# Performance work log

Hardware: AMD Instinct MI355X
Metric: run time of the kernel (lower is better)

Reference implementation:

```python
import jax, jax.numpy as jnp
import numpy as np
import math

D_MODEL = 1024
EXPAND = 2
D_INNER = EXPAND * D_MODEL        # 2048
HEADDIM = 64
NHEADS = D_INNER // HEADDIM       # 32
D_STATE = 128
D_CONV = 4
CHUNK = 128
SEQLEN = 4096
BATCH = 1                         # bidirectional merge in forward hard-codes batch=1
CONV_DIM = D_INNER + 2 * (2 * D_STATE)            # 2560
D_IN_PROJ = 2 * D_INNER + 2 * (2 * D_STATE) + 2 * NHEADS  # 4672
EPS = 1e-5


def silu(x):
    return x * jax.nn.sigmoid(x)


def segsum_exp(a):
    """exp(segsum(a)): out[..., i, j] = exp(sum_{k=j+1..i} a[..., k]) for i>=j else 0."""
    T = a.shape[-1]
    m1 = jnp.tril(jnp.ones((T, T), bool), -1)
    s = jnp.cumsum(jnp.where(m1, a[..., :, None], 0.0), axis=-2)
    m0 = jnp.tril(jnp.ones((T, T), bool))
    return jnp.where(m0, jnp.exp(jnp.where(m0, s, 0.0)), 0.0)


def ssd(x, A, B, C, chunk):
    """x:(b,L,h,p) A:(b,L,h) B,C:(b,L,n) (head dim of size 1 squeezed). L % chunk == 0."""
    b, L, h, p = x.shape
    c = L // chunk
    x = x.reshape(b, c, chunk, h, p)
    A = A.reshape(b, c, chunk, h).transpose(0, 3, 1, 2)   # (b,h,c,l)
    B = B.reshape(b, c, chunk, -1)
    C = C.reshape(b, c, chunk, -1)
    A_cs = jnp.cumsum(A, axis=-1)                          # (b,h,c,l)
    Lmat = segsum_exp(A)                                   # (b,h,c,l,l)
    # intra-chunk (diagonal block) outputs
    Y_diag = jnp.einsum('bcln,bcsn,bhcls,bcshp->bclhp', C, B, Lmat, x)
    # per-chunk states
    decay_states = jnp.exp(A_cs[..., -1:] - A_cs)          # (b,h,c,l)
    states = jnp.einsum('bcln,bhcl,bclhp->bchpn', B, decay_states, x)
    states = jnp.concatenate([jnp.zeros_like(states[:, :1]), states], axis=1)
    # inter-chunk recurrence via segsum over chunk boundaries
    decay_chunk = segsum_exp(jnp.pad(A_cs[..., -1], ((0, 0), (0, 0), (1, 0))))  # (b,h,c+1,c+1)
    new_states = jnp.einsum('bhzc,bchpn->bzhpn', decay_chunk, states)
    states, final_state = new_states[:, :-1], new_states[:, -1]
    Y_off = jnp.einsum('bcln,bchpn,bhcl->bclhp', C, states, jnp.exp(A_cs))
    Y = (Y_diag + Y_off).reshape(b, L, h, p)
    return Y, final_state


def setup_inputs() -> dict:
    key = jax.random.key(0)
    ks = jax.random.split(key, 8)
    s = 0.02
    u = jax.random.normal(ks[0], (BATCH, SEQLEN, D_MODEL), jnp.float32)
    in_proj_w = jax.random.normal(ks[1], (D_IN_PROJ, D_MODEL), jnp.float32) * s
    conv_w = jax.random.normal(ks[2], (CONV_DIM, 1, D_CONV), jnp.float32) * (1.0 / math.sqrt(D_CONV))
    conv_b = jnp.zeros((CONV_DIM,), jnp.float32)
    dt = jnp.exp(jax.random.uniform(ks[3], (NHEADS,)) * (math.log(0.1) - math.log(0.001)) + math.log(0.001))
    dt = jnp.clip(dt, 1e-4)
    dt_bias = dt + jnp.log(-jnp.expm1(-dt))
    A_log = jnp.log(jax.random.uniform(ks[4], (NHEADS,), minval=1.0, maxval=16.0))
    D = jnp.ones((NHEADS,), jnp.float32)
    fc_D_w = jax.random.normal(ks[5], (NHEADS, D_INNER), jnp.float32) * s
    norm_w = jnp.ones((D_INNER,), jnp.float32)
    out_proj_w = jax.random.normal(ks[6], (D_MODEL, D_INNER), jnp.float32) * s
    return dict(u=u, in_proj_w=in_proj_w, conv_w=conv_w, conv_b=conv_b, dt_bias=dt_bias,
                A_log=A_log, D=D, fc_D_w=fc_D_w, norm_w=norm_w, out_proj_w=out_proj_w)


def reference(u, in_proj_w, conv_w, conv_b, dt_bias, A_log, D, fc_D_w, norm_w, out_proj_w):
    b, l, _ = u.shape
    zxbcdt = u @ in_proj_w.T                               # (b,l,D_IN_PROJ)
    z = zxbcdt[..., :D_INNER]
    xBC = zxbcdt[..., D_INNER:D_INNER + CONV_DIM]
    dt = zxbcdt[..., D_INNER + CONV_DIM:]                  # (b,l,2*nheads)
    # fwd heads + time-reversed bwd heads stacked on batch dim
    dt = jnp.concatenate([dt[..., :NHEADS], jnp.flip(dt[..., NHEADS:], axis=1)], axis=0)
    dt = jax.nn.softplus(dt + dt_bias)                     # (2b,l,nheads)
    # depthwise causal conv1d + silu
    xc = jnp.transpose(xBC, (0, 2, 1))                     # (b,CONV_DIM,l)
    xc = jax.lax.conv_general_dilated(xc, conv_w, (1,), [(D_CONV - 1, 0)],
                                      feature_group_count=CONV_DIM,
                                      dimension_numbers=('NCH', 'OIH', 'NCH'))
    xc = xc + conv_b[None, :, None]
    xBC = silu(jnp.transpose(xc, (0, 2, 1)))               # (b,l,CONV_DIM)
    x = xBC[..., :D_INNER]
    BC = xBC[..., D_INNER:]
    x_og = x
    x2 = jnp.concatenate([x, jnp.flip(x, 1)], axis=0)      # (2b,l,d_inner)
    BC = jnp.concatenate([BC[..., :2 * D_STATE], jnp.flip(BC[..., 2 * D_STATE:], 1)], axis=0)
    B = BC[..., :D_STATE]
    C = BC[..., D_STATE:]
    xh = x2.reshape(2 * b, l, NHEADS, HEADDIM)
    A = -jnp.exp(A_log)
    Y, final_state = ssd(xh * dt[..., None], A * dt, B, C, CHUNK)
    y = Y + xh * D[:, None]
    y = y.reshape(2 * b, l, D_INNER)
    # torch.roll(shift=1, dim=1) then zero first step == shift right with zero pad
    y = jnp.concatenate([jnp.zeros_like(y[:, :1]), y[:, :-1]], axis=1)
    y_fw, y_bw = y[:b], jnp.flip(y[b:], 1)
    fd = x_og @ fc_D_w.T + D                               # F.linear(x_og, fc_D.weight, bias=D)
    y = y_fw + y_bw + x_og * jnp.repeat(fd, HEADDIM, axis=-1)
    # gated RMSNorm
    yg = y * silu(z)
    yn = yg * jax.lax.rsqrt(jnp.mean(yg * yg, axis=-1, keepdims=True) + EPS) * norm_w
    return yn @ out_proj_w.T
```

## Files before the change

kernel.cpp:

```cpp
#include <hip/hip_runtime.h>
#include <hip/hip_bf16.h>
#include <math.h>

#define L_SEQ   4096
#define DMODEL  1024
#define DINNER  2048
#define NHEADS  32
#define HEADDIM 64
#define DSTATE  128
#define NCHUNK  32
#define CHUNKL  128
#define CONVDIM 2560
#define DPROJ   4672
#define NPAD1   4736
#define NSPLIT  4096

typedef __hip_bfloat16 bf16;
__device__ __forceinline__ float b2f(bf16 x) { return __bfloat162float(x); }
__device__ __forceinline__ bf16 f2b(float x) { return __float2bfloat16(x); }
__device__ __forceinline__ float sh2f(short s) {
  return __uint_as_float(((unsigned int)(unsigned short)s) << 16);
}
__device__ __forceinline__ short f2bs(float x) {
  bf16 t = __float2bfloat16(x);
  return *reinterpret_cast<short*>(&t);
}

typedef __attribute__((ext_vector_type(8))) short bf16x8v;
typedef __attribute__((ext_vector_type(4))) float f32x4v;

__device__ __forceinline__ float dot8(bf16x8v x, float4 w0, float4 w1) {
  return sh2f(x[0]) * w0.x + sh2f(x[1]) * w0.y + sh2f(x[2]) * w0.z + sh2f(x[3]) * w0.w +
         sh2f(x[4]) * w1.x + sh2f(x[5]) * w1.y + sh2f(x[6]) * w1.z + sh2f(x[7]) * w1.w;
}


__global__ __launch_bounds__(256) void cast2_kernel(
    const float* __restrict__ u, const float* __restrict__ w1,
    bf16* __restrict__ u_bf, bf16* __restrict__ w1_bf) {
  const int NU = (L_SEQ * DMODEL) / 256;
  int bid = blockIdx.x;
  if (bid < NU) {
    int i = bid * 256 + threadIdx.x;
    u_bf[i] = f2b(u[i]);
  } else {
    int i = (bid - NU) * 256 + threadIdx.x;
    w1_bf[i] = (i < DPROJ * DMODEL) ? f2b(w1[i]) : f2b(0.f);
  }
}

__global__ __launch_bounds__(256) void cast_kernel(
    const float* __restrict__ src, bf16* __restrict__ dst, int n_src, int n_tot) {
  int i = blockIdx.x * 256 + threadIdx.x;
  if (i < n_tot) dst[i] = (i < n_src) ? f2b(src[i]) : f2b(0.f);
}

#define G1_K  1024
#define G1_GN 16
#define G1_NT (G1_K / 64)

__global__ __launch_bounds__(512, 2) void gemm1_8ph(
    const bf16* __restrict__ A, const bf16* __restrict__ B, bf16* __restrict__ C) {
  __shared__ bf16 Al[2][2][8192];
  __shared__ bf16 Bl[2][2][8192];
  const int tid = threadIdx.x;
  const int lane = tid & 63;
  const int w = tid >> 6;
  const int wm = w >> 2;
  const int wn = w & 3;
  const int bm = (blockIdx.x / G1_GN) * 256;
  const int bn = (blockIdx.x % G1_GN) * 256;
  const int scol = ((lane & 3) ^ (((lane >> 5) & 1) << 1)) * 8;
  const int cin = ((lane >> 4) * 8) ^ (((lane >> 3) & 1) << 4);
  const int r16 = lane & 15;
  const bf16* Ag = A + (size_t)bm * G1_K;
  const bf16* Bg = B + (size_t)bn * G1_K;

  auto stage = [&](int mat, int tt, int hf) {
    const bf16* g = (mat ? Bg : Ag)
        + (size_t)(hf * 128 + (w >> 1) * 16 + (lane >> 2)) * G1_K
        + tt * 64 + (w & 1) * 32 + scol;
    bf16* d0 = mat ? &Bl[tt & 1][hf][0] : &Al[tt & 1][hf][0];
    __builtin_amdgcn_global_load_lds(
        (const __attribute__((address_space(1))) void*)g,
        (__attribute__((address_space(3))) void*)(d0 + w * 512), 16, 0, 0);
    __builtin_amdgcn_global_load_lds(
        (const __attribute__((address_space(1))) void*)(g + (size_t)64 * G1_K),
        (__attribute__((address_space(3))) void*)(d0 + (8 + w) * 512), 16, 0, 0);
  };

  f32x4v acc[8][4];
#pragma unroll
  for (int i = 0; i < 8; i++)
#pragma unroll
    for (int j = 0; j < 4; j++) acc[i][j] = (f32x4v){0.f, 0.f, 0.f, 0.f};

  stage(0, 0, 0); stage(0, 0, 1); stage(1, 0, 0); stage(1, 0, 1);
  stage(0, 1, 0); stage(0, 1, 1); stage(1, 1, 0);
  asm volatile("s_waitcnt vmcnt(6)" ::: "memory");
  __builtin_amdgcn_s_barrier();
  __builtin_amdgcn_sched_barrier(0);

#pragma unroll 2
  for (int t = 0; t < G1_NT; ++t) {
    const int slot = t & 1;
    const bf16* Ah = &Al[slot][wm][0];
    const bf16* Bh = &Bl[slot][wn >> 1][0];
    const int brb = (wn & 1) * 4;
    bf16x8v a[4][2], b[4][2];
#pragma unroll
    for (int i = 0; i < 4; i++) {
      a[i][0] = *(const bf16x8v*)&Ah[(i * 2 + 0) * 512 + r16 * 32 + cin];
      a[i][1] = *(const bf16x8v*)&Ah[(i * 2 + 1) * 512 + r16 * 32 + cin];
    }
#pragma unroll
    for (int j = 0; j < 2; j++) {
      b[j][0] = *(const bf16x8v*)&Bh[((brb + j) * 2 + 0) * 512 + r16 * 32 + cin];
      b[j][1] = *(const bf16x8v*)&Bh[((brb + j) * 2 + 1) * 512 + r16 * 32 + cin];
    }
    if (t + 1 < G1_NT) stage(1, t + 1, 1);
    __builtin_amdgcn_s_barrier();
    asm volatile("s_waitcnt lgkmcnt(0)" ::: "memory");
    __builtin_amdgcn_s_setprio(1);
#pragma unroll
    for (int i = 0; i < 4; i++)
#pragma unroll
      for (int j = 0; j < 2; j++) {
        acc[i][j] = __builtin_amdgcn_mfma_f32_16x16x32_bf16(a[i][0], b[j][0], acc[i][j], 0, 0, 0);
        acc[i][j] = __builtin_amdgcn_mfma_f32_16x16x32_bf16(a[i][1], b[j][1], acc[i][j], 0, 0, 0);
      }
    __builtin_amdgcn_s_setprio(0);
    __builtin_amdgcn_s_barrier();
#pragma unroll
    for (int j = 2; j < 4; j++) {
      b[j][0] = *(const bf16x8v*)&Bh[((brb + j) * 2 + 0) * 512 + r16 * 32 + cin];
      b[j][1] = *(const bf16x8v*)&Bh[((brb + j) * 2 + 1) * 512 + r16 * 32 + cin];
    }
    __builtin_amdgcn_s_barrier();
    asm volatile("s_waitcnt lgkmcnt(0)" ::: "memory");
    __builtin_amdgcn_s_setprio(1);
#pragma unroll
    for (int i = 0; i < 4; i++)
#pragma unroll
      for (int j = 2; j < 4; j++) {
        acc[i][j] = __builtin_amdgcn_mfma_f32_16x16x32_bf16(a[i][0], b[j][0], acc[i][j], 0, 0, 0);
        acc[i][j] = __builtin_amdgcn_mfma_f32_16x16x32_bf16(a[i][1], b[j][1], acc[i][j], 0, 0, 0);
      }
    __builtin_amdgcn_s_setprio(0);
    __builtin_amdgcn_s_barrier();
#pragma unroll
    for (int i = 0; i < 4; i++) {
      a[i][0] = *(const bf16x8v*)&Ah[((4 + i) * 2 + 0) * 512 + r16 * 32 + cin];
      a[i][1] = *(const bf16x8v*)&Ah[((4 + i) * 2 + 1) * 512 + r16 * 32 + cin];
    }
    if (t + 2 < G1_NT) stage(1, t + 2, 0);
    __builtin_amdgcn_s_barrier();
    asm volatile("s_waitcnt lgkmcnt(0)" ::: "memory");
    __builtin_amdgcn_s_setprio(1);
#pragma unroll
    for (int i = 0; i < 4; i++)
#pragma unroll
      for (int j = 2; j < 4; j++) {
        acc[4 + i][j] = __builtin_amdgcn_mfma_f32_16x16x32_bf16(a[i][0], b[j][0], acc[4 + i][j], 0, 0, 0);
        acc[4 + i][j] = __builtin_amdgcn_mfma_f32_16x16x32_bf16(a[i][1], b[j][1], acc[4 + i][j], 0, 0, 0);
      }
    __builtin_amdgcn_s_setprio(0);
    __builtin_amdgcn_s_barrier();
    if (t + 2 < G1_NT) { stage(0, t + 2, 0); stage(0, t + 2, 1); }
    __builtin_amdgcn_s_barrier();
    __builtin_amdgcn_s_setprio(1);
#pragma unroll
    for (int i = 0; i < 4; i++)
#pragma unroll
      for (int j = 0; j < 2; j++) {
        acc[4 + i][j] = __builtin_amdgcn_mfma_f32_16x16x32_bf16(a[i][0], b[j][0], acc[4 + i][j], 0, 0, 0);
        acc[4 + i][j] = __builtin_amdgcn_mfma_f32_16x16x32_bf16(a[i][1], b[j][1], acc[4 + i][j], 0, 0, 0);
      }
    __builtin_amdgcn_s_setprio(0);
    if (t < G1_NT - 2)       asm volatile("s_waitcnt vmcnt(6)" ::: "memory");
    else if (t == G1_NT - 2) asm volatile("s_waitcnt vmcnt(0)" ::: "memory");
    __builtin_amdgcn_s_barrier();
    __builtin_amdgcn_sched_barrier(0);
  }

  const int quad = lane >> 4;
  const int cn = lane & 15;
#pragma unroll
  for (int i = 0; i < 8; i++)
#pragma unroll
    for (int j = 0; j < 4; j++) {
      int col = bn + wn * 64 + j * 16 + cn;
      if (col < DPROJ) {
#pragma unroll
        for (int r = 0; r < 4; r++) {
          int row = bm + wm * 128 + i * 16 + quad * 4 + r;
          C[(size_t)row * DPROJ + col] = f2b(acc[i][j][r]);
        }
      }
    }
}

template <typename TC>
__global__ __launch_bounds__(256) void gemm_mfma(
    const bf16* __restrict__ A, int lda,
    const bf16* __restrict__ B, int ldb,
    TC* __restrict__ C, int ldc,
    int N, int K, int gridM, int gridN, int swz) {
  __shared__ short As[128][32];
  __shared__ short Bs[128][32];
  int tid = threadIdx.x;
  int lane = tid & 63;
  int w = tid >> 6;
  int wr = w >> 1, wc = w & 1;
  int bid = blockIdx.x;
  int bm, bn;
  if (swz) {
    int mst = gridM >> 3;
    int xk = bid & 7, q = bid >> 3;
    bm = (xk + 8 * (q % mst)) * 128;
    bn = (q / mst) * 128;
  } else {
    bm = (bid / gridN) * 128;
    bn = (bid % gridN) * 128;
  }
  f32x4v acc[4][4];
#pragma unroll
  for (int i = 0; i < 4; i++)
#pragma unroll
    for (int j = 0; j < 4; j++) acc[i][j] = (f32x4v){0.f, 0.f, 0.f, 0.f};

  const bf16* Ab = A + (size_t)(bm + w * 32 + (lane >> 2)) * lda + (lane & 3) * 8;
  const bf16* Bb = B + (size_t)(bn + w * 32 + (lane >> 2)) * ldb + (lane & 3) * 8;

  for (int k0 = 0; k0 < K; k0 += 32) {
    __builtin_amdgcn_global_load_lds(
        (const __attribute__((address_space(1))) void*)(Ab + k0),
        (__attribute__((address_space(3))) void*)&As[w * 32][0], 16, 0, 0);
    __builtin_amdgcn_global_load_lds(
        (const __attribute__((address_space(1))) void*)(Ab + (size_t)16 * lda + k0),
        (__attribute__((address_space(3))) void*)&As[w * 32 + 16][0], 16, 0, 0);
    __builtin_amdgcn_global_load_lds(
        (const __attribute__((address_space(1))) void*)(Bb + k0),
        (__attribute__((address_space(3))) void*)&Bs[w * 32][0], 16, 0, 0);
    __builtin_amdgcn_global_load_lds(
        (const __attribute__((address_space(1))) void*)(Bb + (size_t)16 * ldb + k0),
        (__attribute__((address_space(3))) void*)&Bs[w * 32 + 16][0], 16, 0, 0);
    __syncthreads();
    bf16x8v af[4], bv[4];
#pragma unroll
    for (int i = 0; i < 4; i++)
      af[i] = *(const bf16x8v*)&As[wr * 64 + i * 16 + (lane & 15)][(lane >> 4) * 8];
#pragma unroll
    for (int j = 0; j < 4; j++)
      bv[j] = *(const bf16x8v*)&Bs[wc * 64 + j * 16 + (lane & 15)][(lane >> 4) * 8];
#pragma unroll
    for (int i = 0; i < 4; i++)
#pragma unroll
      for (int j = 0; j < 4; j++)
        acc[i][j] = __builtin_amdgcn_mfma_f32_16x16x32_bf16(af[i], bv[j], acc[i][j], 0, 0, 0);
    __syncthreads();
  }
  int quad = lane >> 4;
  int cn = lane & 15;
#pragma unroll
  for (int i = 0; i < 4; i++) {
#pragma unroll
    for (int j = 0; j < 4; j++) {
      int col = bn + wc * 64 + j * 16 + cn;
      if (col < N) {
#pragma unroll
        for (int r = 0; r < 4; r++) {
          int row = bm + wr * 64 + i * 16 + quad * 4 + r;
          float v = acc[i][j][r];
          if constexpr (sizeof(TC) == 2) C[(size_t)row * ldc + col] = f2b(v);
          else                           C[(size_t)row * ldc + col] = v;
        }
      }
    }
  }
}

__global__ __launch_bounds__(256) void fc_kernel(
    const bf16* __restrict__ xbc, const float* __restrict__ Wf,
    const float* __restrict__ Dp, float* __restrict__ fd) {
  int lane = threadIdx.x & 63;
  int w = threadIdx.x >> 6;
  int t0 = blockIdx.x * 4;
  int h = lane & 31;
  int g = lane >> 5;
  int k0 = w * 512 + g * 256;
  const float* wr = Wf + (size_t)h * DINNER + k0;
  const bf16* xr = xbc + (size_t)t0 * CONVDIM + k0;
  float a0 = 0.f, a1 = 0.f, a2 = 0.f, a3 = 0.f;
#pragma unroll 4
  for (int k = 0; k < 256; k += 8) {
    float4 w0 = *(const float4*)(wr + k);
    float4 w1 = *(const float4*)(wr + k + 4);
    bf16x8v x0 = *(const bf16x8v*)(xr + k);
    bf16x8v x1 = *(const bf16x8v*)(xr + CONVDIM + k);
    bf16x8v x2 = *(const bf16x8v*)(xr + 2 * CONVDIM + k);
    bf16x8v x3 = *(const bf16x8v*)(xr + 3 * CONVDIM + k);
    a0 += dot8(x0, w0, w1);
    a1 += dot8(x1, w0, w1);
    a2 += dot8(x2, w0, w1);
    a3 += dot8(x3, w0, w1);
  }
  a0 += __shfl_down(a0, 32);
  a1 += __shfl_down(a1, 32);
  a2 += __shfl_down(a2, 32);
  a3 += __shfl_down(a3, 32);
  __shared__ float red[4][4][32];
  if (lane < 32) {
    red[w][0][h] = a0; red[w][1][h] = a1; red[w][2][h] = a2; red[w][3][h] = a3;
  }
  __syncthreads();
  int tid = threadIdx.x;
  if (tid < 128) {
    int tt = tid >> 5;
    int hh = tid & 31;
    float s = red[0][tt][hh] + red[1][tt][hh] + red[2][tt][hh] + red[3][tt][hh];
    fd[(t0 + tt) * NHEADS + hh] = s + Dp[hh];
  }
}

#define CONV_BLOCKS ((L_SEQ / 4) * CONVDIM / 256)
__global__ __launch_bounds__(256) void conv_dt_kernel(
    const bf16* __restrict__ zx, const float* __restrict__ conv_w,
    const float* __restrict__ conv_b, bf16* __restrict__ xbc,
    const float* __restrict__ dt_bias, float* __restrict__ dt2) {
  int bid = blockIdx.x;
  if (bid < CONV_BLOCKS) {
    int idx = bid * 256 + threadIdx.x;
    int ch = idx % CONVDIM;
    int t0 = (idx / CONVDIM) * 4;
    const bf16* col = zx + DINNER + ch;
    float w0 = conv_w[ch * 4 + 0], w1 = conv_w[ch * 4 + 1];
    float w2 = conv_w[ch * 4 + 2], w3 = conv_w[ch * 4 + 3];
    float bsv = conv_b[ch];
    float x[7];
#pragma unroll
    for (int i = 0; i < 7; i++) {
      int t = t0 - 3 + i;
      x[i] = (t >= 0) ? b2f(col[(size_t)t * DPROJ]) : 0.f;
    }
#pragma unroll
    for (int j = 0; j < 4; j++) {
      float acc = bsv + w0 * x[j] + w1 * x[j + 1] + w2 * x[j + 2] + w3 * x[j + 3];
      xbc[(size_t)(t0 + j) * CONVDIM + ch] = f2b(acc / (1.f + __expf(-acc)));
    }
  } else {
    int idx = (bid - CONV_BLOCKS) * 256 + threadIdx.x;
    int h = idx % NHEADS;
    int t = (idx / NHEADS) % L_SEQ;
    int b = idx / (NHEADS * L_SEQ);
    float v;
    if (b == 0) v = b2f(zx[(size_t)t * DPROJ + 4608 + h]);
    else        v = b2f(zx[(size_t)(L_SEQ - 1 - t) * DPROJ + 4608 + NHEADS + h]);
    v += dt_bias[h];
    dt2[idx] = (v > 20.f) ? v : log1pf(expf(v));
  }
}

__global__ __launch_bounds__(256) void gmat_kernel(
    const bf16* __restrict__ xbc, bf16* __restrict__ G) {
  __shared__ bf16 Cs[32][136];
  __shared__ bf16 Bs[128][136];
  int blk = blockIdx.x;
  int quarter = blk & 3;
  int bc = blk >> 2;
  int b = bc / NCHUNK, c = bc % NCHUNK;
  int l0 = quarter * 32;
  int tid = threadIdx.x;
  int lane = tid & 63;
  int w = tid >> 6;
  int bofs = b ? 2304 : 2048;
  int cofs = b ? 2432 : 2176;
  for (int o = tid; o < CHUNKL * DSTATE / 8; o += 256) {
    int s = o >> 4;
    int n8 = (o & 15) * 8;
    int t = b ? (L_SEQ - 1 - (c * CHUNKL + s)) : (c * CHUNKL + s);
    *(bf16x8v*)&Bs[s][n8] = *(const bf16x8v*)&xbc[(size_t)t * CONVDIM + bofs + n8];
  }
  for (int o = tid; o < 32 * DSTATE / 8; o += 256) {
    int l = o >> 4;
    int n8 = (o & 15) * 8;
    int t = b ? (L_SEQ - 1 - (c * CHUNKL + l0 + l)) : (c * CHUNKL + l0 + l);
    *(bf16x8v*)&Cs[l][n8] = *(const bf16x8v*)&xbc[(size_t)t * CONVDIM + cofs + n8];
  }
  __syncthreads();
  if (w > quarter) return;
  f32x4v acc[2][2];
#pragma unroll
  for (int i = 0; i < 2; i++)
#pragma unroll
    for (int j = 0; j < 2; j++) acc[i][j] = (f32x4v){0.f, 0.f, 0.f, 0.f};
#pragma unroll
  for (int k0 = 0; k0 < 128; k0 += 32) {
    bf16x8v a0 = *(const bf16x8v*)&Cs[(lane & 15)][(lane >> 4) * 8 + k0];
    bf16x8v a1 = *(const bf16x8v*)&Cs[16 + (lane & 15)][(lane >> 4) * 8 + k0];
#pragma unroll
    for (int j = 0; j < 2; j++) {
      bf16x8v bv = *(const bf16x8v*)&Bs[(2 * w + j) * 16 + (lane & 15)][(lane >> 4) * 8 + k0];
      acc[0][j] = __builtin_amdgcn_mfma_f32_16x16x32_bf16(a0, bv, acc[0][j], 0, 0, 0);
      acc[1][j] = __builtin_amdgcn_mfma_f32_16x16x32_bf16(a1, bv, acc[1][j], 0, 0, 0);
    }
  }
  int quad = lane >> 4, cn = lane & 15;
  bf16* Gb = G + (size_t)bc * CHUNKL * CHUNKL;
#pragma unroll
  for (int i = 0; i < 2; i++)
#pragma unroll
    for (int j = 0; j < 2; j++)
#pragma unroll
      for (int r = 0; r < 4; r++) {
        int l = l0 + i * 16 + quad * 4 + r;
        int s = (2 * w + j) * 16 + cn;
        Gb[l * CHUNKL + s] = f2b(acc[i][j][r]);
      }
}

__global__ __launch_bounds__(256) void chunk_kernel(
    const bf16* __restrict__ xbc, const float* __restrict__ dt2,
    const float* __restrict__ A_log,
    bf16* __restrict__ states, float* __restrict__ csum) {
  int gid = blockIdx.x;
  int h = gid % NHEADS;
  int bc = gid / NHEADS;
  int c = bc % NCHUNK, b = bc / NCHUNK;
  int tid = threadIdx.x;
  int lane = tid & 63;
  int w = tid >> 6;
  __shared__ bf16 BdT[128][136];
  __shared__ bf16 xdtT[64][136];
  __shared__ float acs[CHUNKL];
  __shared__ float dtl[CHUNKL];
  __shared__ float decays[CHUNKL];
  if (tid < CHUNKL)
    dtl[tid] = dt2[((size_t)b * L_SEQ + c * CHUNKL + tid) * NHEADS + h];
  __syncthreads();
  if (tid == 0) {
    float Ah = -__expf(A_log[h]);
    float s = 0.f;
    for (int l = 0; l < CHUNKL; l++) { s += Ah * dtl[l]; acs[l] = s; }
    csum[gid] = __expf(s);
  }
  __syncthreads();
  if (tid < CHUNKL) decays[tid] = __expf(acs[CHUNKL - 1] - acs[tid]);
  for (int o = tid; o < CHUNKL * HEADDIM / 8; o += 256) {
    int s = o & 127;
    int p8 = (o >> 7) * 8;
    int t = b ? (L_SEQ - 1 - (c * CHUNKL + s)) : (c * CHUNKL + s);
    bf16x8v xv = *(const bf16x8v*)&xbc[(size_t)t * CONVDIM + h * HEADDIM + p8];
    float d = dtl[s];
#pragma unroll
    for (int j = 0; j < 8; j++) xdtT[p8 + j][s] = f2b(sh2f(xv[j]) * d);
  }
  __syncthreads();
  for (int o = tid; o < CHUNKL * CHUNKL / 8; o += 256) {
    int l = o & 127;
    int n8 = (o >> 7) * 8;
    int t = b ? (L_SEQ - 1 - (c * CHUNKL + l)) : (c * CHUNKL + l);
    bf16x8v bv = *(const bf16x8v*)&xbc[(size_t)t * CONVDIM + (b ? 2304 : 2048) + n8];
    float d = decays[l];
#pragma unroll
    for (int j = 0; j < 8; j++) BdT[n8 + j][l] = f2b(sh2f(bv[j]) * d);
  }
  __syncthreads();
  f32x4v accS[8];
#pragma unroll
  for (int j = 0; j < 8; j++) accS[j] = (f32x4v){0.f, 0.f, 0.f, 0.f};
#pragma unroll
  for (int k0 = 0; k0 < 128; k0 += 32) {
    bf16x8v av = *(const bf16x8v*)&xdtT[w * 16 + (lane & 15)][(lane >> 4) * 8 + k0];
#pragma unroll
    for (int j = 0; j < 8; j++) {
      bf16x8v bv = *(const bf16x8v*)&BdT[j * 16 + (lane & 15)][(lane >> 4) * 8 + k0];
      accS[j] = __builtin_amdgcn_mfma_f32_16x16x32_bf16(av, bv, accS[j], 0, 0, 0);
    }
  }
  int quad = lane >> 4, cn = lane & 15;
  bf16* st = states + (size_t)gid * (HEADDIM * DSTATE);
#pragma unroll
  for (int j = 0; j < 8; j++)
#pragma unroll
    for (int r = 0; r < 4; r++) {
      int p = w * 16 + quad * 4 + r;
      int n = j * 16 + cn;
      st[p * DSTATE + n] = f2b(accS[j][r]);
    }
}

__global__ __launch_bounds__(256) void scan_kernel(
    bf16* __restrict__ states, const float* __restrict__ csum) {
  int idx = blockIdx.x * 256 + threadIdx.x;
  int n = idx % DSTATE;
  int p = (idx / DSTATE) % HEADDIM;
  int h = (idx / (DSTATE * HEADDIM)) % NHEADS;
  int b = idx / (DSTATE * HEADDIM * NHEADS);
  size_t base = ((size_t)(b * NCHUNK) * NHEADS + h) * (HEADDIM * DSTATE) + p * DSTATE + n;
  const size_t cstride = (size_t)NHEADS * HEADDIM * DSTATE;
  float tmp[NCHUNK], cv[NCHUNK];
#pragma unroll
  for (int c = 0; c < NCHUNK; c++) tmp[c] = b2f(states[base + c * cstride]);
#pragma unroll
  for (int c = 0; c < NCHUNK; c++) cv[c] = csum[(b * NCHUNK + c) * NHEADS + h];
  float S = 0.f;
#pragma unroll
  for (int c = 0; c < NCHUNK; c++) {
    states[base + c * cstride] = f2b(S);
    S = cv[c] * S + tmp[c];
  }
}

__global__ __launch_bounds__(256) void yoff_kernel(
    const bf16* __restrict__ xbc, const float* __restrict__ dt2,
    const float* __restrict__ A_log, const bf16* __restrict__ G,
    const bf16* __restrict__ states, const float* __restrict__ Dp,
    bf16* __restrict__ Y) {
  int gid = blockIdx.x;
  int h = gid % NHEADS;
  int bc = gid / NHEADS;
  int c = bc % NCHUNK, b = bc / NCHUNK;
  int tid = threadIdx.x;
  int lane = tid & 63;
  int w = tid >> 6;
  __shared__ bf16 WB[128][136];
  __shared__ bf16 SX[64][136];
  __shared__ float acs[CHUNKL];
  __shared__ float dtl[CHUNKL];
  __shared__ float eAl[CHUNKL];
  if (tid < CHUNKL)
    dtl[tid] = dt2[((size_t)b * L_SEQ + c * CHUNKL + tid) * NHEADS + h];
  __syncthreads();
  if (tid == 0) {
    float Ah = -__expf(A_log[h]);
    float s = 0.f;
    for (int l = 0; l < CHUNKL; l++) { s += Ah * dtl[l]; acs[l] = s; }
  }
  __syncthreads();
  if (tid < CHUNKL) eAl[tid] = __expf(acs[tid]);
  for (int o = tid; o < CHUNKL * HEADDIM / 8; o += 256) {
    int s = o & 127;
    int p8 = (o >> 7) * 8;
    int t = b ? (L_SEQ - 1 - (c * CHUNKL + s)) : (c * CHUNKL + s);
    bf16x8v xv = *(const bf16x8v*)&xbc[(size_t)t * CONVDIM + h * HEADDIM + p8];
    float d = dtl[s];
#pragma unroll
    for (int j = 0; j < 8; j++) SX[p8 + j][s] = f2b(sh2f(xv[j]) * d);
  }
  {
    const bf16* Gb = G + (size_t)bc * CHUNKL * CHUNKL;
    for (int o = tid; o < CHUNKL * CHUNKL / 8; o += 256) {
      int l = o >> 4;
      int s8 = (o & 15) * 8;
      bf16x8v g = *(const bf16x8v*)&Gb[l * CHUNKL + s8];
      float al = acs[l];
      bf16x8v wv;
#pragma unroll
      for (int j = 0; j < 8; j++) {
        int s = s8 + j;
        float e = (s <= l) ? sh2f(g[j]) * __expf(al - acs[s]) : 0.f;
        wv[j] = f2bs(e);
      }
      *(bf16x8v*)&WB[l][s8] = wv;
    }
  }
  __syncthreads();
  f32x4v accY[2][4];
#pragma unroll
  for (int i = 0; i < 2; i++)
#pragma unroll
    for (int j = 0; j < 4; j++) accY[i][j] = (f32x4v){0.f, 0.f, 0.f, 0.f};
#pragma unroll
  for (int k0 = 0; k0 < 128; k0 += 32) {
    bf16x8v a0 = *(const bf16x8v*)&WB[w * 32 + (lane & 15)][(lane >> 4) * 8 + k0];
    bf16x8v a1 = *(const bf16x8v*)&WB[w * 32 + 16 + (lane & 15)][(lane >> 4) * 8 + k0];
#pragma unroll
    for (int j = 0; j < 4; j++) {
      bf16x8v bv = *(const bf16x8v*)&SX[j * 16 + (lane & 15)][(lane >> 4) * 8 + k0];
      accY[0][j] = __builtin_amdgcn_mfma_f32_16x16x32_bf16(a0, bv, accY[0][j], 0, 0, 0);
      accY[1][j] = __builtin_amdgcn_mfma_f32_16x16x32_bf16(a1, bv, accY[1][j], 0, 0, 0);
    }
  }
  __syncthreads();
  {
    int cofs = b ? 2432 : 2176;
    for (int o = tid; o < CHUNKL * DSTATE / 8; o += 256) {
      int l = o >> 4;
      int n8 = (o & 15) * 8;
      int t = b ? (L_SEQ - 1 - (c * CHUNKL + l)) : (c * CHUNKL + l);
      bf16x8v cv = *(const bf16x8v*)&xbc[(size_t)t * CONVDIM + cofs + n8];
      float e = eAl[l];
      bf16x8v ov;
#pragma unroll
      for (int j = 0; j < 8; j++) ov[j] = f2bs(sh2f(cv[j]) * e);
      *(bf16x8v*)&WB[l][n8] = ov;
    }
    const bf16* stp = states + (size_t)gid * (HEADDIM * DSTATE);
    for (int o = tid; o < HEADDIM * DSTATE / 8; o += 256) {
      int p = o >> 4;
      int n8 = (o & 15) * 8;
      *(bf16x8v*)&SX[p][n8] = *(const bf16x8v*)&stp[o * 8];
    }
  }
  __syncthreads();
#pragma unroll
  for (int k0 = 0; k0 < 128; k0 += 32) {
    bf16x8v a0 = *(const bf16x8v*)&WB[w * 32 + (lane & 15)][(lane >> 4) * 8 + k0];
    bf16x8v a1 = *(const bf16x8v*)&WB[w * 32 + 16 + (lane & 15)][(lane >> 4) * 8 + k0];
#pragma unroll
    for (int j = 0; j < 4; j++) {
      bf16x8v bv = *(const bf16x8v*)&SX[j * 16 + (lane & 15)][(lane >> 4) * 8 + k0];
      accY[0][j] = __builtin_amdgcn_mfma_f32_16x16x32_bf16(a0, bv, accY[0][j], 0, 0, 0);
      accY[1][j] = __builtin_amdgcn_mfma_f32_16x16x32_bf16(a1, bv, accY[1][j], 0, 0, 0);
    }
  }
  int quad = lane >> 4, cn = lane & 15;
  float Dh = Dp[h];
#pragma unroll
  for (int i = 0; i < 2; i++)
#pragma unroll
    for (int j = 0; j < 4; j++)
#pragma unroll
      for (int r = 0; r < 4; r++) {
        int l = w * 32 + i * 16 + quad * 4 + r;
        int p = j * 16 + cn;
        int t = b ? (L_SEQ - 1 - (c * CHUNKL + l)) : (c * CHUNKL + l);
        float xv = b2f(xbc[(size_t)t * CONVDIM + h * HEADDIM + p]);
        size_t yi = ((size_t)b * L_SEQ + c * CHUNKL + l) * DINNER + h * HEADDIM + p;
        Y[yi] = f2b(accY[i][j][r] + xv * Dh);
      }
}

__global__ __launch_bounds__(256) void combine_kernel(
    const bf16* __restrict__ Y, const bf16* __restrict__ xbc,
    const bf16* __restrict__ zx, const float* __restrict__ fd,
    const float* __restrict__ norm_w, bf16* __restrict__ yn) {
  int t = blockIdx.x;
  int tid = threadIdx.x;
  int j8 = tid * 8;
  float yf[8], yb[8];
#pragma unroll
  for (int j = 0; j < 8; j++) { yf[j] = 0.f; yb[j] = 0.f; }
  if (t >= 1) {
    bf16x8v v = *(const bf16x8v*)&Y[(size_t)(t - 1) * DINNER + j8];
#pragma unroll
    for (int j = 0; j < 8; j++) yf[j] = sh2f(v[j]);
  }
  if (t <= L_SEQ - 2) {
    bf16x8v v = *(const bf16x8v*)&Y[((size_t)L_SEQ + (L_SEQ - 2 - t)) * DINNER + j8];
#pragma unroll
    for (int j = 0; j < 8; j++) yb[j] = sh2f(v[j]);
  }
  bf16x8v xogv = *(const bf16x8v*)&xbc[(size_t)t * CONVDIM + j8];
  bf16x8v zv = *(const bf16x8v*)&zx[(size_t)t * DPROJ + j8];
  float fdv = fd[t * NHEADS + (j8 >> 6)];
  float yg[8];
  float ss = 0.f;
#pragma unroll
  for (int j = 0; j < 8; j++) {
    float y = yf[j] + yb[j] + sh2f(xogv[j]) * fdv;
    float z = sh2f(zv[j]);
    float g = y * (z / (1.f + __expf(-z)));
    yg[j] = g;
    ss += g * g;
  }
#pragma unroll
  for (int off = 32; off > 0; off >>= 1) ss += __shfl_down(ss, off);
  __shared__ float red[4];
  if ((tid & 63) == 0) red[tid >> 6] = ss;
  __syncthreads();
  float tot = red[0] + red[1] + red[2] + red[3];
  float scale = rsqrtf(tot / (float)DINNER + 1e-5f);
  float4 nw0 = *(const float4*)&norm_w[j8];
  float4 nw1 = *(const float4*)&norm_w[j8 + 4];
  bf16x8v ov;
  ov[0] = f2bs(yg[0] * scale * nw0.x);
  ov[1] = f2bs(yg[1] * scale * nw0.y);
  ov[2] = f2bs(yg[2] * scale * nw0.z);
  ov[3] = f2bs(yg[3] * scale * nw0.w);
  ov[4] = f2bs(yg[4] * scale * nw1.x);
  ov[5] = f2bs(yg[5] * scale * nw1.y);
  ov[6] = f2bs(yg[6] * scale * nw1.z);
  ov[7] = f2bs(yg[7] * scale * nw1.w);
  *(bf16x8v*)&yn[(size_t)t * DINNER + j8] = ov;
}

extern "C" void kernel_launch(void* const* d_in, const int* in_sizes, int n_in,
                              void* d_out, int out_size, void* d_ws, size_t ws_size,
                              hipStream_t stream) {
  const float* u         = (const float*)d_in[0];
  const float* in_proj_w = (const float*)d_in[1];
  const float* conv_w    = (const float*)d_in[2];
  const float* conv_b    = (const float*)d_in[3];
  const float* dt_bias   = (const float*)d_in[4];
  const float* A_log     = (const float*)d_in[5];
  const float* Dp        = (const float*)d_in[6];
  const float* fc_D_w    = (const float*)d_in[7];
  const float* norm_w    = (const float*)d_in[8];
  const float* out_proj_w= (const float*)d_in[9];
  float* out = (float*)d_out;

  char* base = (char*)d_ws;
  bf16*  zx  = (bf16*)base;  base += (size_t)L_SEQ * DPROJ * 2;
  bf16*  xbc = (bf16*)base;  base += (size_t)L_SEQ * CONVDIM * 2;
  float* dt2 = (float*)base; base += (size_t)2 * L_SEQ * NHEADS * 4;
  bf16*  G   = (bf16*)base;  base += (size_t)2 * NCHUNK * CHUNKL * CHUNKL * 4;
  bf16*  Yb  = (bf16*)base;  base += (size_t)2 * L_SEQ * DINNER * 4;
  bf16*  stb = (bf16*)base;  base += (size_t)2 * NCHUNK * NHEADS * HEADDIM * DSTATE * 4;
  float* cs  = (float*)base; base += (size_t)2 * NCHUNK * NHEADS * 4;
  bf16*  u_bf   = (bf16*)Yb;
  bf16*  w1p_bf = (bf16*)((char*)Yb + 9437184);
  bf16*  w2_bf  = (bf16*)G;
  bf16*  yn     = (bf16*)stb;
  float* fd     = (float*)((char*)stb + 33554432);

  cast2_kernel<<<(L_SEQ * DMODEL + NPAD1 * DMODEL) / 256, 256, 0, stream>>>(
      u, in_proj_w, u_bf, w1p_bf);
  gemm1_8ph<<<(L_SEQ / 256) * G1_GN, 512, 0, stream>>>(u_bf, w1p_bf, zx);
  gemm_mfma<bf16><<<(L_SEQ / 128) * ((NPAD1 - NSPLIT) / 128), 256, 0, stream>>>(
      u_bf, DMODEL, w1p_bf + (size_t)NSPLIT * DMODEL, DMODEL,
      zx + NSPLIT, DPROJ, DPROJ - NSPLIT, DMODEL,
      L_SEQ / 128, (NPAD1 - NSPLIT) / 128, 0);
  conv_dt_kernel<<<CONV_BLOCKS + (2 * L_SEQ * NHEADS) / 256, 256, 0, stream>>>(
      zx, conv_w, conv_b, xbc, dt_bias, dt2);
  gmat_kernel<<<2 * NCHUNK * 4, 256, 0, stream>>>(xbc, G);
  chunk_kernel<<<2 * NCHUNK * NHEADS, 256, 0, stream>>>(
      xbc, dt2, A_log, stb, cs);
  scan_kernel<<<(2 * NHEADS * HEADDIM * DSTATE) / 256, 256, 0, stream>>>(stb, cs);
  yoff_kernel<<<2 * NCHUNK * NHEADS, 256, 0, stream>>>(
      xbc, dt2, A_log, G, stb, Dp, Yb);
  cast_kernel<<<(DMODEL * DINNER + 255) / 256, 256, 0, stream>>>(
      out_proj_w, w2_bf, DMODEL * DINNER, DMODEL * DINNER);
  fc_kernel<<<L_SEQ / 4, 256, 0, stream>>>(xbc, fc_D_w, Dp, fd);
  combine_kernel<<<L_SEQ, 256, 0, stream>>>(Yb, xbc, zx, fd, norm_w, yn);
  gemm_mfma<float><<<(L_SEQ / 128) * (DMODEL / 128), 256, 0, stream>>>(
      yn, DINNER, w2_bf, DINNER, out, DMODEL, DMODEL, DINNER,
      L_SEQ / 128, DMODEL / 128, 1);
}
```

Baseline: 403.5 us.

## Split yoff kernel rows across two blocks, skip masked causal tiles, parallel cumsum

The yoff kernel is launched with twice as many blocks, each handling 64 of the 128 chunk rows, which halves the WB shared buffer and the per-wave accumulators. The causal (lower-triangular) structure is used to skip loading G and computing exponentials for fully masked 8-wide segments, and to break out of the intra-chunk MFMA loop once k passes the wave's last row. The serial single-thread cumulative sum over dt is replaced by a wavefront shuffle-based prefix scan. In exchange, each block still reloads the dt vector, the SX tile and the state tile, so that global traffic is duplicated across the two halves.

```diff
diff --git a/kernel.cpp b/kernel.cpp
--- a/kernel.cpp
+++ b/kernel.cpp
@@ -517,14 +517,17 @@
     const float* __restrict__ A_log, const bf16* __restrict__ G,
     const bf16* __restrict__ states, const float* __restrict__ Dp,
     bf16* __restrict__ Y) {
-  int gid = blockIdx.x;
+  int blk = blockIdx.x;
+  int half = blk & 1;
+  int gid = blk >> 1;
   int h = gid % NHEADS;
   int bc = gid / NHEADS;
   int c = bc % NCHUNK, b = bc / NCHUNK;
+  int l0 = half * 64;
   int tid = threadIdx.x;
   int lane = tid & 63;
   int w = tid >> 6;
-  __shared__ bf16 WB[128][136];
+  __shared__ bf16 WB[64][136];
   __shared__ bf16 SX[64][136];
   __shared__ float acs[CHUNKL];
   __shared__ float dtl[CHUNKL];
@@ -532,10 +535,18 @@
   if (tid < CHUNKL)
     dtl[tid] = dt2[((size_t)b * L_SEQ + c * CHUNKL + tid) * NHEADS + h];
   __syncthreads();
-  if (tid == 0) {
+  if (tid < 64) {
     float Ah = -__expf(A_log[h]);
-    float s = 0.f;
-    for (int l = 0; l < CHUNKL; l++) { s += Ah * dtl[l]; acs[l] = s; }
+    float v0 = Ah * dtl[2 * tid];
+    float v1 = Ah * dtl[2 * tid + 1];
+    float s = v0 + v1;
+#pragma unroll
+    for (int off = 1; off < 64; off <<= 1) {
+      float t = __shfl_up(s, off);
+      if (tid >= off) s += t;
+    }
+    acs[2 * tid]     = s - v1;
+    acs[2 * tid + 1] = s;
   }
   __syncthreads();
   if (tid < CHUNKL) eAl[tid] = __expf(acs[tid]);
@@ -550,43 +561,48 @@
   }
   {
     const bf16* Gb = G + (size_t)bc * CHUNKL * CHUNKL;
-    for (int o = tid; o < CHUNKL * CHUNKL / 8; o += 256) {
-      int l = o >> 4;
+    for (int o = tid; o < 64 * CHUNKL / 8; o += 256) {
+      int ll = o >> 4;
+      int l = l0 + ll;
       int s8 = (o & 15) * 8;
-      bf16x8v g = *(const bf16x8v*)&Gb[l * CHUNKL + s8];
-      float al = acs[l];
       bf16x8v wv;
-#pragma unroll
-      for (int j = 0; j < 8; j++) {
-        int s = s8 + j;
-        float e = (s <= l) ? sh2f(g[j]) * __expf(al - acs[s]) : 0.f;
-        wv[j] = f2bs(e);
+      if (s8 > l) {
+#pragma unroll
+        for (int j = 0; j < 8; j++) wv[j] = 0;
+      } else {
+        bf16x8v g = *(const bf16x8v*)&Gb[l * CHUNKL + s8];
+        float al = acs[l];
+#pragma unroll
+        for (int j = 0; j < 8; j++) {
+          int s = s8 + j;
+          float e = (s <= l) ? sh2f(g[j]) * __expf(al - acs[s]) : 0.f;
+          wv[j] = f2bs(e);
+        }
       }
-      *(bf16x8v*)&WB[l][s8] = wv;
-    }
-  }
-  __syncthreads();
-  f32x4v accY[2][4];
-#pragma unroll
-  for (int i = 0; i < 2; i++)
-#pragma unroll
-    for (int j = 0; j < 4; j++) accY[i][j] = (f32x4v){0.f, 0.f, 0.f, 0.f};
+      *(bf16x8v*)&WB[ll][s8] = wv;
+    }
+  }
+  __syncthreads();
+  f32x4v accY[4];
+#pragma unroll
+  for (int j = 0; j < 4; j++) accY[j] = (f32x4v){0.f, 0.f, 0.f, 0.f};
+  const int kcap = l0 + w * 16 + 15;
 #pragma unroll
   for (int k0 = 0; k0 < 128; k0 += 32) {
-    bf16x8v a0 = *(const bf16x8v*)&WB[w * 32 + (lane & 15)][(lane >> 4) * 8 + k0];
-    bf16x8v a1 = *(const bf16x8v*)&WB[w * 32 + 16 + (lane & 15)][(lane >> 4) * 8 + k0];
+    if (k0 > kcap) break;
+    bf16x8v a0 = *(const bf16x8v*)&WB[w * 16 + (lane & 15)][(lane >> 4) * 8 + k0];
 #pragma unroll
     for (int j = 0; j < 4; j++) {
       bf16x8v bv = *(const bf16x8v*)&SX[j * 16 + (lane & 15)][(lane >> 4) * 8 + k0];
-      accY[0][j] = __builtin_amdgcn_mfma_f32_16x16x32_bf16(a0, bv, accY[0][j], 0, 0, 0);
-      accY[1][j] = __builtin_amdgcn_mfma_f32_16x16x32_bf16(a1, bv, accY[1][j], 0, 0, 0);
+      accY[j] = __builtin_amdgcn_mfma_f32_16x16x32_bf16(a0, bv, accY[j], 0, 0, 0);
     }
   }
   __syncthreads();
   {
     int cofs = b ? 2432 : 2176;
-    for (int o = tid; o < CHUNKL * DSTATE / 8; o += 256) {
-      int l = o >> 4;
+    for (int o = tid; o < 64 * DSTATE / 8; o += 256) {
+      int ll = o >> 4;
+      int l = l0 + ll;
       int n8 = (o & 15) * 8;
       int t = b ? (L_SEQ - 1 - (c * CHUNKL + l)) : (c * CHUNKL + l);
       bf16x8v cv = *(const bf16x8v*)&xbc[(size_t)t * CONVDIM + cofs + n8];
@@ -594,7 +610,7 @@
       bf16x8v ov;
 #pragma unroll
       for (int j = 0; j < 8; j++) ov[j] = f2bs(sh2f(cv[j]) * e);
-      *(bf16x8v*)&WB[l][n8] = ov;
+      *(bf16x8v*)&WB[ll][n8] = ov;
     }
     const bf16* stp = states + (size_t)gid * (HEADDIM * DSTATE);
     for (int o = tid; o < HEADDIM * DSTATE / 8; o += 256) {
@@ -606,30 +622,26 @@
   __syncthreads();
 #pragma unroll
   for (int k0 = 0; k0 < 128; k0 += 32) {
-    bf16x8v a0 = *(const bf16x8v*)&WB[w * 32 + (lane & 15)][(lane >> 4) * 8 + k0];
-    bf16x8v a1 = *(const bf16x8v*)&WB[w * 32 + 16 + (lane & 15)][(lane >> 4) * 8 + k0];
+    bf16x8v a0 = *(const bf16x8v*)&WB[w * 16 + (lane & 15)][(lane >> 4) * 8 + k0];
 #pragma unroll
     for (int j = 0; j < 4; j++) {
       bf16x8v bv = *(const bf16x8v*)&SX[j * 16 + (lane & 15)][(lane >> 4) * 8 + k0];
-      accY[0][j] = __builtin_amdgcn_mfma_f32_16x16x32_bf16(a0, bv, accY[0][j], 0, 0, 0);
-      accY[1][j] = __builtin_amdgcn_mfma_f32_16x16x32_bf16(a1, bv, accY[1][j], 0, 0, 0);
+      accY[j] = __builtin_amdgcn_mfma_f32_16x16x32_bf16(a0, bv, accY[j], 0, 0, 0);
     }
   }
   int quad = lane >> 4, cn = lane & 15;
   float Dh = Dp[h];
 #pragma unroll
-  for (int i = 0; i < 2; i++)
-#pragma unroll
-    for (int j = 0; j < 4; j++)
-#pragma unroll
-      for (int r = 0; r < 4; r++) {
-        int l = w * 32 + i * 16 + quad * 4 + r;
-        int p = j * 16 + cn;
-        int t = b ? (L_SEQ - 1 - (c * CHUNKL + l)) : (c * CHUNKL + l);
-        float xv = b2f(xbc[(size_t)t * CONVDIM + h * HEADDIM + p]);
-        size_t yi = ((size_t)b * L_SEQ + c * CHUNKL + l) * DINNER + h * HEADDIM + p;
-        Y[yi] = f2b(accY[i][j][r] + xv * Dh);
-      }
+  for (int j = 0; j < 4; j++)
+#pragma unroll
+    for (int r = 0; r < 4; r++) {
+      int l = l0 + w * 16 + quad * 4 + r;
+      int p = j * 16 + cn;
+      int t = b ? (L_SEQ - 1 - (c * CHUNKL + l)) : (c * CHUNKL + l);
+      float xv = b2f(xbc[(size_t)t * CONVDIM + h * HEADDIM + p]);
+      size_t yi = ((size_t)b * L_SEQ + c * CHUNKL + l) * DINNER + h * HEADDIM + p;
+      Y[yi] = f2b(accY[j][r] + xv * Dh);
+    }
 }
 
 __global__ __launch_bounds__(256) void combine_kernel(
@@ -728,7 +740,7 @@
   chunk_kernel<<<2 * NCHUNK * NHEADS, 256, 0, stream>>>(
       xbc, dt2, A_log, stb, cs);
   scan_kernel<<<(2 * NHEADS * HEADDIM * DSTATE) / 256, 256, 0, stream>>>(stb, cs);
-  yoff_kernel<<<2 * NCHUNK * NHEADS, 256, 0, stream>>>(
+  yoff_kernel<<<2 * NCHUNK * NHEADS * 2, 256, 0, stream>>>(
       xbc, dt2, A_log, G, stb, Dp, Yb);
   cast_kernel<<<(DMODEL * DINNER + 255) / 256, 256, 0, stream>>>(
       out_proj_w, w2_bf, DMODEL * DINNER, DMODEL * DINNER);
```

New measurement: 405.2 us. Within noise of the previous version (+0.4%).

## Parallelize chunk cumsum, prefetch C/states into registers, skip masked tiles

Applied to the files above, without the earlier changes.

Replaces the single-thread serial cumsum over the chunk with a 64-lane wavefront shuffle scan. C and chunk states are loaded into registers early, so their global latency overlaps the intra-chunk work, then written to LDS after the first GEMM. Reads of G and exp work for strictly upper-triangular 8-wide blocks are skipped, and MFMA k-steps above each wave's diagonal are skipped. This adds register pressure (12 extra 128-bit vectors per thread), which may lower occupancy.

```diff
diff --git a/kernel.cpp b/kernel.cpp
--- a/kernel.cpp
+++ b/kernel.cpp
@@ -532,13 +532,39 @@
   if (tid < CHUNKL)
     dtl[tid] = dt2[((size_t)b * L_SEQ + c * CHUNKL + tid) * NHEADS + h];
   __syncthreads();
-  if (tid == 0) {
+  if (tid < 64) {
     float Ah = -__expf(A_log[h]);
-    float s = 0.f;
-    for (int l = 0; l < CHUNKL; l++) { s += Ah * dtl[l]; acs[l] = s; }
+    float v0 = Ah * dtl[2 * tid];
+    float v1 = Ah * dtl[2 * tid + 1];
+    float s = v0 + v1;
+#pragma unroll
+    for (int off = 1; off < 64; off <<= 1) {
+      float t = __shfl_up(s, off);
+      if (tid >= off) s += t;
+    }
+    acs[2 * tid]     = s - v1;
+    acs[2 * tid + 1] = s;
   }
   __syncthreads();
   if (tid < CHUNKL) eAl[tid] = __expf(acs[tid]);
+  bf16x8v ce_r[8], st_r[4];
+  {
+    int cofs = b ? 2432 : 2176;
+#pragma unroll
+    for (int it = 0; it < 8; it++) {
+      int o = tid + it * 256;
+      int l = o >> 4;
+      int n8 = (o & 15) * 8;
+      int t = b ? (L_SEQ - 1 - (c * CHUNKL + l)) : (c * CHUNKL + l);
+      ce_r[it] = *(const bf16x8v*)&xbc[(size_t)t * CONVDIM + cofs + n8];
+    }
+    const bf16* stp = states + (size_t)gid * (HEADDIM * DSTATE);
+#pragma unroll
+    for (int it = 0; it < 4; it++) {
+      int o = tid + it * 256;
+      st_r[it] = *(const bf16x8v*)&stp[o * 8];
+    }
+  }
   for (int o = tid; o < CHUNKL * HEADDIM / 8; o += 256) {
     int s = o & 127;
     int p8 = (o >> 7) * 8;
@@ -553,14 +579,19 @@
     for (int o = tid; o < CHUNKL * CHUNKL / 8; o += 256) {
       int l = o >> 4;
       int s8 = (o & 15) * 8;
-      bf16x8v g = *(const bf16x8v*)&Gb[l * CHUNKL + s8];
-      float al = acs[l];
       bf16x8v wv;
-#pragma unroll
-      for (int j = 0; j < 8; j++) {
-        int s = s8 + j;
-        float e = (s <= l) ? sh2f(g[j]) * __expf(al - acs[s]) : 0.f;
-        wv[j] = f2bs(e);
+      if (s8 > l) {
+#pragma unroll
+        for (int j = 0; j < 8; j++) wv[j] = 0;
+      } else {
+        bf16x8v g = *(const bf16x8v*)&Gb[l * CHUNKL + s8];
+        float al = acs[l];
+#pragma unroll
+        for (int j = 0; j < 8; j++) {
+          int s = s8 + j;
+          float e = (s <= l) ? sh2f(g[j]) * __expf(al - acs[s]) : 0.f;
+          wv[j] = f2bs(e);
+        }
       }
       *(bf16x8v*)&WB[l][s8] = wv;
     }
@@ -573,6 +604,7 @@
     for (int j = 0; j < 4; j++) accY[i][j] = (f32x4v){0.f, 0.f, 0.f, 0.f};
 #pragma unroll
   for (int k0 = 0; k0 < 128; k0 += 32) {
+    if (k0 > w * 32 + 31) break;
     bf16x8v a0 = *(const bf16x8v*)&WB[w * 32 + (lane & 15)][(lane >> 4) * 8 + k0];
     bf16x8v a1 = *(const bf16x8v*)&WB[w * 32 + 16 + (lane & 15)][(lane >> 4) * 8 + k0];
 #pragma unroll
@@ -584,23 +616,23 @@
   }
   __syncthreads();
   {
-    int cofs = b ? 2432 : 2176;
-    for (int o = tid; o < CHUNKL * DSTATE / 8; o += 256) {
+#pragma unroll
+    for (int it = 0; it < 8; it++) {
+      int o = tid + it * 256;
       int l = o >> 4;
       int n8 = (o & 15) * 8;
-      int t = b ? (L_SEQ - 1 - (c * CHUNKL + l)) : (c * CHUNKL + l);
-      bf16x8v cv = *(const bf16x8v*)&xbc[(size_t)t * CONVDIM + cofs + n8];
       float e = eAl[l];
       bf16x8v ov;
 #pragma unroll
-      for (int j = 0; j < 8; j++) ov[j] = f2bs(sh2f(cv[j]) * e);
+      for (int j = 0; j < 8; j++) ov[j] = f2bs(sh2f(ce_r[it][j]) * e);
       *(bf16x8v*)&WB[l][n8] = ov;
     }
-    const bf16* stp = states + (size_t)gid * (HEADDIM * DSTATE);
-    for (int o = tid; o < HEADDIM * DSTATE / 8; o += 256) {
+#pragma unroll
+    for (int it = 0; it < 4; it++) {
+      int o = tid + it * 256;
       int p = o >> 4;
       int n8 = (o & 15) * 8;
-      *(bf16x8v*)&SX[p][n8] = *(const bf16x8v*)&stp[o * 8];
+      *(bf16x8v*)&SX[p][n8] = st_r[it];
     }
   }
   __syncthreads();
```

Result: no change. 398.1 us (-1.3%).
